# Kernel optimization log

Hardware: AMD Instinct MI355X
Metric: run time of the kernel (lower is better)

The kernel has to match this reference:

```python
import jax, jax.numpy as jnp
import numpy as np

N = 50000          # nodes
E = 800000         # edges (avg degree 16)
IN_C = 3
HEADS = 4
NUM_GRAPHS = 8
NUM_CLASSES = 10


def setup_inputs() -> dict:
    key = jax.random.key(0)
    ks = jax.random.split(key, 12)
    x = jax.random.normal(ks[0], (N, IN_C), jnp.float32)
    edge_index = jax.random.randint(ks[1], (2, E), 0, N, dtype=jnp.int64)
    batch = jnp.sort(jax.random.randint(ks[2], (N,), 0, NUM_GRAPHS, dtype=jnp.int64))

    def glorot(k, shape, fan):
        return jax.random.normal(k, shape, jnp.float32) * np.float32(1.0 / np.sqrt(fan))

    return {
        "x": x, "edge_index": edge_index, "batch": batch,
        "fc0_w": glorot(ks[3], (IN_C, 16), IN_C), "fc0_b": jnp.zeros((16,), jnp.float32),
        "u1": glorot(ks[4], (16, HEADS), 16), "c1": jnp.zeros((HEADS,), jnp.float32),
        "w1": glorot(ks[5], (16, HEADS * 32), 16), "b1": jnp.zeros((32,), jnp.float32),
        "u2": glorot(ks[6], (32, HEADS), 32), "c2": jnp.zeros((HEADS,), jnp.float32),
        "w2": glorot(ks[7], (32, HEADS * 64), 32), "b2": jnp.zeros((64,), jnp.float32),
        "fc1_w": glorot(ks[8], (64, NUM_CLASSES), 64), "fc1_b": jnp.zeros((NUM_CLASSES,), jnp.float32),
    }


def feast_conv(x, src, dst, u, c, w, b, heads, out_c):
    """FeaStConv (t_inv=True): per-edge head softmax on (x_j - x_i), mean aggregation."""
    n = x.shape[0]
    # soft-assignment over heads: [E, H]
    q = jax.nn.softmax((x[src] - x[dst]) @ u + c, axis=-1)
    # transform at node level, then gather per edge: [E, H, out_c]
    xw = (x @ w).reshape(n, heads, out_c)
    msg = jnp.einsum('eh,ehc->ec', q, xw[src])           # [E, out_c]
    agg = jax.ops.segment_sum(msg, dst, num_segments=n)  # sum over incoming edges
    cnt = jax.ops.segment_sum(jnp.ones((src.shape[0],), x.dtype), dst, num_segments=n)
    return agg / jnp.maximum(cnt, 1.0)[:, None] + b


def global_mean_pool(x, batch, num_graphs):
    s = jax.ops.segment_sum(x, batch, num_segments=num_graphs)
    cnt = jax.ops.segment_sum(jnp.ones((x.shape[0],), x.dtype), batch, num_segments=num_graphs)
    return s / jnp.maximum(cnt, 1.0)[:, None]


def reference(x, edge_index, batch, fc0_w, fc0_b, u1, c1, w1, b1, u2, c2, w2, b2, fc1_w, fc1_b):
    src, dst = edge_index[0], edge_index[1]   # x_j = x[src], x_i = x[dst]
    h = jax.nn.relu(x @ fc0_w + fc0_b)                              # [N, 16]
    h = jax.nn.relu(feast_conv(h, src, dst, u1, c1, w1, b1, HEADS, 32))  # [N, 32]
    h = jax.nn.relu(feast_conv(h, src, dst, u2, c2, w2, b2, HEADS, 64))  # [N, 64]
    g = global_mean_pool(h, batch, NUM_GRAPHS)                      # [G, 64]
    # dropout is identity in eval mode
    return g @ fc1_w + fc1_b                                        # [G, num_classes]
```

## Files before the change

kernel.cpp:

```cpp
#include <hip/hip_runtime.h>

#define N_NODES 50000
#define N_EDGES 800000
#define HEADS 4
#define NUM_GRAPHS 8

#define EBLK ((N_EDGES + 255) / 256)
#define NBLK ((N_NODES + 255) / 256)

__global__ __launch_bounds__(256) void hist_fc0_kernel(
    const int* __restrict__ dst, int* __restrict__ deg, int* __restrict__ off,
    const float* __restrict__ x,
    const float* __restrict__ fc0_w, const float* __restrict__ fc0_b,
    const float* __restrict__ u1,
    float* __restrict__ h0, float* __restrict__ P1) {
  if (blockIdx.x < EBLK) {
    int e = blockIdx.x * 256 + threadIdx.x;
    if (e < N_EDGES) off[e] = atomicAdd(&deg[dst[e]], 1);
    return;
  }
  __shared__ float sW0[3 * 16];
  __shared__ float sB0[16];
  __shared__ float sU[16 * 4];
  for (int i = threadIdx.x; i < 48; i += 256) sW0[i] = fc0_w[i];
  for (int i = threadIdx.x; i < 16; i += 256) sB0[i] = fc0_b[i];
  for (int i = threadIdx.x; i < 64; i += 256) sU[i] = u1[i];
  __syncthreads();
  int n = (blockIdx.x - EBLK) * 256 + threadIdx.x;
  if (n >= N_NODES) return;
  float x0 = x[n * 3 + 0], x1 = x[n * 3 + 1], x2 = x[n * 3 + 2];
  float h[16];
#pragma unroll
  for (int j = 0; j < 16; j++) {
    float v = x0 * sW0[0 * 16 + j] + x1 * sW0[1 * 16 + j] + x2 * sW0[2 * 16 + j] + sB0[j];
    h[j] = fmaxf(v, 0.f);
    h0[(size_t)n * 16 + j] = h[j];
  }
  float p0 = 0.f, p1 = 0.f, p2 = 0.f, p3 = 0.f;
#pragma unroll
  for (int j = 0; j < 16; j++) {
    p0 += h[j] * sU[j * 4 + 0];
    p1 += h[j] * sU[j * 4 + 1];
    p2 += h[j] * sU[j * 4 + 2];
    p3 += h[j] * sU[j * 4 + 3];
  }
  reinterpret_cast<float4*>(P1)[n] = make_float4(p0, p1, p2, p3);
}

__global__ __launch_bounds__(256) void alloc_kernel(const int* __restrict__ deg,
                                                    int* __restrict__ gctr,
                                                    int* __restrict__ rowstart) {
  int i = blockIdx.x * blockDim.x + threadIdx.x;
  int lane = threadIdx.x & 63;
  int d = (i < N_NODES) ? deg[i] : 0;
  int pre = d;
#pragma unroll
  for (int offd = 1; offd < 64; offd <<= 1) {
    int v = __shfl_up(pre, offd, 64);
    if (lane >= offd) pre += v;
  }
  int total = __shfl(pre, 63, 64);
  int base = 0;
  if (lane == 63) base = atomicAdd(gctr, total);
  base = __shfl(base, 63, 64);
  if (i < N_NODES) rowstart[i] = base + pre - d;
}

__global__ __launch_bounds__(256) void scatter_kernel(const int* __restrict__ src,
                                                      const int* __restrict__ dst,
                                                      const int* __restrict__ rowstart,
                                                      const int* __restrict__ off,
                                                      int* __restrict__ src_perm) {
  int e = blockIdx.x * blockDim.x + threadIdx.x;
  if (e >= N_EDGES) return;
  src_perm[rowstart[dst[e]] + off[e]] = src[e];
}

__device__ __forceinline__ float4 edge_q(float4 Ps, float b0, float b1, float b2, float b3) {
  float l0 = Ps.x + b0, l1 = Ps.y + b1, l2 = Ps.z + b2, l3 = Ps.w + b3;
  float m = fmaxf(fmaxf(l0, l1), fmaxf(l2, l3));
  float e0 = __expf(l0 - m), e1 = __expf(l1 - m), e2 = __expf(l2 - m), e3 = __expf(l3 - m);
  float inv = 1.f / (e0 + e1 + e2 + e3);
  return make_float4(e0 * inv, e1 * inv, e2 * inv, e3 * inv);
}

__global__ __launch_bounds__(256) void agg1_kernel(
    const int* __restrict__ rowstart, const int* __restrict__ deg,
    const int* __restrict__ src_perm,
    const float* __restrict__ P1, const float* __restrict__ c1,
    const float* __restrict__ h0,
    float* __restrict__ A) {
  int wave = threadIdx.x >> 6;
  int lane = threadIdx.x & 63;
  int g = lane >> 4;
  int j = lane & 15;
  int node = blockIdx.x * 4 + wave;
  if (node >= N_NODES) return;
  float4 Pd = reinterpret_cast<const float4*>(P1)[node];
  float b0 = c1[0] - Pd.x, b1 = c1[1] - Pd.y, b2 = c1[2] - Pd.z, b3 = c1[3] - Pd.w;
  int e0 = rowstart[node];
  int e1 = e0 + deg[node];
  const float4* P4 = reinterpret_cast<const float4*>(P1);
  float a0 = 0.f, a1 = 0.f, a2 = 0.f, a3 = 0.f;
  int p = e0;
  for (; p + 16 <= e1; p += 16) {
    int sA = src_perm[p + 0 + g];
    int sB = src_perm[p + 4 + g];
    int sC = src_perm[p + 8 + g];
    int sD = src_perm[p + 12 + g];
    float4 PA = P4[sA];
    float4 PB = P4[sB];
    float4 PC = P4[sC];
    float4 PD = P4[sD];
    float fA = h0[(size_t)sA * 16 + j];
    float fB = h0[(size_t)sB * 16 + j];
    float fC = h0[(size_t)sC * 16 + j];
    float fD = h0[(size_t)sD * 16 + j];
    float4 qA = edge_q(PA, b0, b1, b2, b3);
    float4 qB = edge_q(PB, b0, b1, b2, b3);
    float4 qC = edge_q(PC, b0, b1, b2, b3);
    float4 qD = edge_q(PD, b0, b1, b2, b3);
    a0 += qA.x * fA + qB.x * fB + qC.x * fC + qD.x * fD;
    a1 += qA.y * fA + qB.y * fB + qC.y * fC + qD.y * fD;
    a2 += qA.z * fA + qB.z * fB + qC.z * fC + qD.z * fD;
    a3 += qA.w * fA + qB.w * fB + qC.w * fC + qD.w * fD;
  }
  for (; p + 4 <= e1; p += 4) {
    int s = src_perm[p + g];
    float4 Ps = P4[s];
    float f = h0[(size_t)s * 16 + j];
    float4 q = edge_q(Ps, b0, b1, b2, b3);
    a0 += q.x * f; a1 += q.y * f; a2 += q.z * f; a3 += q.w * f;
  }
  int rem = e1 - p;
  if (g < rem) {
    int s = src_perm[p + g];
    float4 Ps = P4[s];
    float f = h0[(size_t)s * 16 + j];
    float4 q = edge_q(Ps, b0, b1, b2, b3);
    a0 += q.x * f; a1 += q.y * f; a2 += q.z * f; a3 += q.w * f;
  }
  a0 += __shfl_xor(a0, 16, 64); a0 += __shfl_xor(a0, 32, 64);
  a1 += __shfl_xor(a1, 16, 64); a1 += __shfl_xor(a1, 32, 64);
  a2 += __shfl_xor(a2, 16, 64); a2 += __shfl_xor(a2, 32, 64);
  a3 += __shfl_xor(a3, 16, 64); a3 += __shfl_xor(a3, 32, 64);
  float o = (g == 0) ? a0 : (g == 1) ? a1 : (g == 2) ? a2 : a3;
  A[(size_t)node * 64 + lane] = o;
}

__global__ __launch_bounds__(256) void agg2_kernel(
    const int* __restrict__ rowstart, const int* __restrict__ deg,
    const int* __restrict__ src_perm,
    const float* __restrict__ P2, const float* __restrict__ c2,
    const float* __restrict__ h1,
    float* __restrict__ A) {
  int wave = threadIdx.x >> 6;
  int lane = threadIdx.x & 63;
  int g = lane >> 5;
  int j = lane & 31;
  int node = blockIdx.x * 4 + wave;
  if (node >= N_NODES) return;
  float4 Pd = reinterpret_cast<const float4*>(P2)[node];
  float b0 = c2[0] - Pd.x, b1 = c2[1] - Pd.y, b2 = c2[2] - Pd.z, b3 = c2[3] - Pd.w;
  int e0 = rowstart[node];
  int e1 = e0 + deg[node];
  const float4* P4 = reinterpret_cast<const float4*>(P2);
  float a0 = 0.f, a1 = 0.f, a2 = 0.f, a3 = 0.f;
  int p = e0;
  for (; p + 8 <= e1; p += 8) {
    int sA = src_perm[p + 0 + g];
    int sB = src_perm[p + 2 + g];
    int sC = src_perm[p + 4 + g];
    int sD = src_perm[p + 6 + g];
    float4 PA = P4[sA];
    float4 PB = P4[sB];
    float4 PC = P4[sC];
    float4 PD = P4[sD];
    float fA = h1[(size_t)sA * 32 + j];
    float fB = h1[(size_t)sB * 32 + j];
    float fC = h1[(size_t)sC * 32 + j];
    float fD = h1[(size_t)sD * 32 + j];
    float4 qA = edge_q(PA, b0, b1, b2, b3);
    float4 qB = edge_q(PB, b0, b1, b2, b3);
    float4 qC = edge_q(PC, b0, b1, b2, b3);
    float4 qD = edge_q(PD, b0, b1, b2, b3);
    a0 += qA.x * fA + qB.x * fB + qC.x * fC + qD.x * fD;
    a1 += qA.y * fA + qB.y * fB + qC.y * fC + qD.y * fD;
    a2 += qA.z * fA + qB.z * fB + qC.z * fC + qD.z * fD;
    a3 += qA.w * fA + qB.w * fB + qC.w * fC + qD.w * fD;
  }
  for (; p + 2 <= e1; p += 2) {
    int s = src_perm[p + g];
    float4 Ps = P4[s];
    float f = h1[(size_t)s * 32 + j];
    float4 q = edge_q(Ps, b0, b1, b2, b3);
    a0 += q.x * f; a1 += q.y * f; a2 += q.z * f; a3 += q.w * f;
  }
  int rem = e1 - p;
  if (g < rem) {
    int s = src_perm[p + g];
    float4 Ps = P4[s];
    float f = h1[(size_t)s * 32 + j];
    float4 q = edge_q(Ps, b0, b1, b2, b3);
    a0 += q.x * f; a1 += q.y * f; a2 += q.z * f; a3 += q.w * f;
  }
  a0 += __shfl_xor(a0, 32, 64);
  a1 += __shfl_xor(a1, 32, 64);
  a2 += __shfl_xor(a2, 32, 64);
  a3 += __shfl_xor(a3, 32, 64);
  float oa = (g == 0) ? a0 : a1;
  float ob = (g == 0) ? a2 : a3;
  A[(size_t)node * 128 + lane] = oa;
  A[(size_t)node * 128 + 64 + lane] = ob;
}

__global__ __launch_bounds__(256) void gemm1_kernel(
    const int* __restrict__ deg, const float* __restrict__ A,
    const float* __restrict__ w1, const float* __restrict__ b1,
    const float* __restrict__ u2,
    float* __restrict__ h1, float* __restrict__ P2) {
  __shared__ float sB[64 * 32];
  __shared__ float sU[32 * 4];
  for (int i = threadIdx.x; i < 64 * 32; i += 256) {
    int hj = i / 32, c = i % 32;
    sB[i] = w1[(hj % 16) * 128 + (hj / 16) * 32 + c];
  }
  for (int i = threadIdx.x; i < 128; i += 256) sU[i] = u2[i];
  __syncthreads();
  const float4* sB4 = reinterpret_cast<const float4*>(sB);
  int c4 = threadIdx.x & 7;
  int g = threadIdx.x >> 3;
  int n0 = blockIdx.x * 64 + g * 2;
  int n1 = n0 + 1;
  int na = min(n0, N_NODES - 1);
  int nb = min(n1, N_NODES - 1);
  const float4* A0 = reinterpret_cast<const float4*>(A + (size_t)na * 64);
  const float4* A1 = reinterpret_cast<const float4*>(A + (size_t)nb * 64);
  float4 bc = reinterpret_cast<const float4*>(b1)[c4];
  float4 acc0 = {0, 0, 0, 0}, acc1 = {0, 0, 0, 0};
#pragma unroll 2
  for (int k4 = 0; k4 < 16; k4++) {
    float4 a0 = A0[k4];
    float4 a1 = A1[k4];
    float4 w0 = sB4[(4 * k4 + 0) * 8 + c4];
    float4 wv1 = sB4[(4 * k4 + 1) * 8 + c4];
    float4 w2v = sB4[(4 * k4 + 2) * 8 + c4];
    float4 w3 = sB4[(4 * k4 + 3) * 8 + c4];
    acc0.x += a0.x * w0.x + a0.y * wv1.x + a0.z * w2v.x + a0.w * w3.x;
    acc0.y += a0.x * w0.y + a0.y * wv1.y + a0.z * w2v.y + a0.w * w3.y;
    acc0.z += a0.x * w0.z + a0.y * wv1.z + a0.z * w2v.z + a0.w * w3.z;
    acc0.w += a0.x * w0.w + a0.y * wv1.w + a0.z * w2v.w + a0.w * w3.w;
    acc1.x += a1.x * w0.x + a1.y * wv1.x + a1.z * w2v.x + a1.w * w3.x;
    acc1.y += a1.x * w0.y + a1.y * wv1.y + a1.z * w2v.y + a1.w * w3.y;
    acc1.z += a1.x * w0.z + a1.y * wv1.z + a1.z * w2v.z + a1.w * w3.z;
    acc1.w += a1.x * w0.w + a1.y * wv1.w + a1.z * w2v.w + a1.w * w3.w;
  }
  float inv0 = 1.f / fmaxf((float)deg[na], 1.f);
  float inv1 = 1.f / fmaxf((float)deg[nb], 1.f);
  float4 o0 = {fmaxf(acc0.x * inv0 + bc.x, 0.f), fmaxf(acc0.y * inv0 + bc.y, 0.f),
               fmaxf(acc0.z * inv0 + bc.z, 0.f), fmaxf(acc0.w * inv0 + bc.w, 0.f)};
  float4 o1 = {fmaxf(acc1.x * inv1 + bc.x, 0.f), fmaxf(acc1.y * inv1 + bc.y, 0.f),
               fmaxf(acc1.z * inv1 + bc.z, 0.f), fmaxf(acc1.w * inv1 + bc.w, 0.f)};
  if (n0 < N_NODES) reinterpret_cast<float4*>(h1 + (size_t)n0 * 32)[c4] = o0;
  if (n1 < N_NODES) reinterpret_cast<float4*>(h1 + (size_t)n1 * 32)[c4] = o1;
  float pa[4] = {0, 0, 0, 0}, pb[4] = {0, 0, 0, 0};
#pragma unroll
  for (int k = 0; k < 4; k++) {
    int c = 4 * c4 + k;
    float v0 = k == 0 ? o0.x : k == 1 ? o0.y : k == 2 ? o0.z : o0.w;
    float v1 = k == 0 ? o1.x : k == 1 ? o1.y : k == 2 ? o1.z : o1.w;
#pragma unroll
    for (int hh = 0; hh < 4; hh++) {
      pa[hh] += v0 * sU[c * 4 + hh];
      pb[hh] += v1 * sU[c * 4 + hh];
    }
  }
#pragma unroll
  for (int msk = 1; msk <= 4; msk <<= 1) {
#pragma unroll
    for (int hh = 0; hh < 4; hh++) {
      pa[hh] += __shfl_xor(pa[hh], msk, 64);
      pb[hh] += __shfl_xor(pb[hh], msk, 64);
    }
  }
  if (c4 == 0) {
    if (n0 < N_NODES)
      reinterpret_cast<float4*>(P2)[n0] = make_float4(pa[0], pa[1], pa[2], pa[3]);
    if (n1 < N_NODES)
      reinterpret_cast<float4*>(P2)[n1] = make_float4(pb[0], pb[1], pb[2], pb[3]);
  }
}

__global__ __launch_bounds__(256) void gemm2_kernel(
    const int* __restrict__ deg, const float* __restrict__ A,
    const float* __restrict__ w2, const float* __restrict__ b2,
    float* __restrict__ h2) {
  __shared__ float sB[128 * 64];
  for (int i = threadIdx.x; i < 128 * 64; i += 256) {
    int hj = i / 64, c = i % 64;
    sB[i] = w2[(hj % 32) * 256 + (hj / 32) * 64 + c];
  }
  __syncthreads();
  const float4* sB4 = reinterpret_cast<const float4*>(sB);
  int c4 = threadIdx.x & 15;
  int g = threadIdx.x >> 4;
  int n0 = blockIdx.x * 32 + g * 2;
  int n1 = n0 + 1;
  int na = min(n0, N_NODES - 1);
  int nb = min(n1, N_NODES - 1);
  const float4* A0 = reinterpret_cast<const float4*>(A + (size_t)na * 128);
  const float4* A1 = reinterpret_cast<const float4*>(A + (size_t)nb * 128);
  float4 bc = reinterpret_cast<const float4*>(b2)[c4];
  float4 acc0 = {0, 0, 0, 0}, acc1 = {0, 0, 0, 0};
#pragma unroll 2
  for (int k4 = 0; k4 < 32; k4++) {
    float4 a0 = A0[k4];
    float4 a1 = A1[k4];
    float4 w0 = sB4[(4 * k4 + 0) * 16 + c4];
    float4 wv1 = sB4[(4 * k4 + 1) * 16 + c4];
    float4 w2v = sB4[(4 * k4 + 2) * 16 + c4];
    float4 w3 = sB4[(4 * k4 + 3) * 16 + c4];
    acc0.x += a0.x * w0.x + a0.y * wv1.x + a0.z * w2v.x + a0.w * w3.x;
    acc0.y += a0.x * w0.y + a0.y * wv1.y + a0.z * w2v.y + a0.w * w3.y;
    acc0.z += a0.x * w0.z + a0.y * wv1.z + a0.z * w2v.z + a0.w * w3.z;
    acc0.w += a0.x * w0.w + a0.y * wv1.w + a0.z * w2v.w + a0.w * w3.w;
    acc1.x += a1.x * w0.x + a1.y * wv1.x + a1.z * w2v.x + a1.w * w3.x;
    acc1.y += a1.x * w0.y + a1.y * wv1.y + a1.z * w2v.y + a1.w * w3.y;
    acc1.z += a1.x * w0.z + a1.y * wv1.z + a1.z * w2v.z + a1.w * w3.z;
    acc1.w += a1.x * w0.w + a1.y * wv1.w + a1.z * w2v.w + a1.w * w3.w;
  }
  if (n0 < N_NODES) {
    float inv = 1.f / fmaxf((float)deg[n0], 1.f);
    float4 o = {fmaxf(acc0.x * inv + bc.x, 0.f), fmaxf(acc0.y * inv + bc.y, 0.f),
                fmaxf(acc0.z * inv + bc.z, 0.f), fmaxf(acc0.w * inv + bc.w, 0.f)};
    reinterpret_cast<float4*>(h2 + (size_t)n0 * 64)[c4] = o;
  }
  if (n1 < N_NODES) {
    float inv = 1.f / fmaxf((float)deg[n1], 1.f);
    float4 o = {fmaxf(acc1.x * inv + bc.x, 0.f), fmaxf(acc1.y * inv + bc.y, 0.f),
                fmaxf(acc1.z * inv + bc.z, 0.f), fmaxf(acc1.w * inv + bc.w, 0.f)};
    reinterpret_cast<float4*>(h2 + (size_t)n1 * 64)[c4] = o;
  }
}

#define POOL_CHUNK 64
__global__ __launch_bounds__(256) void pool_kernel(
    const float* __restrict__ h2, const int* __restrict__ batch,
    float* __restrict__ gsum, float* __restrict__ gcnt) {
  int grp = threadIdx.x / 64;
  int c = threadIdx.x % 64;
  int n0 = (blockIdx.x * 4 + grp) * POOL_CHUNK;
  int n1 = min(n0 + POOL_CHUNK, N_NODES);
  if (n0 >= N_NODES) return;
  float acc = 0.f;
  float cacc = 0.f;
  int curg = batch[n0];
  for (int n = n0; n < n1; n++) {
    int g = batch[n];
    float v = h2[(size_t)n * 64 + c];
    if (g != curg) {
      atomicAdd(&gsum[curg * 64 + c], acc);
      if (c == 0) atomicAdd(&gcnt[curg], cacc);
      acc = 0.f;
      cacc = 0.f;
      curg = g;
    }
    acc += v;
    cacc += 1.f;
  }
  atomicAdd(&gsum[curg * 64 + c], acc);
  if (c == 0) atomicAdd(&gcnt[curg], cacc);
}

__global__ __launch_bounds__(128) void head_kernel(
    const float* __restrict__ gsum, const float* __restrict__ gcnt,
    const float* __restrict__ fc1_w, const float* __restrict__ fc1_b,
    float* __restrict__ out) {
  int t = threadIdx.x;
  if (t >= NUM_GRAPHS * 10) return;
  int g = t / 10, k = t % 10;
  float inv = 1.f / fmaxf(gcnt[g], 1.f);
  float s = fc1_b[k];
#pragma unroll
  for (int c = 0; c < 64; c++) s += gsum[g * 64 + c] * inv * fc1_w[c * 10 + k];
  out[g * 10 + k] = s;
}

extern "C" void kernel_launch(void* const* d_in, const int* in_sizes, int n_in,
                              void* d_out, int out_size, void* d_ws, size_t ws_size,
                              hipStream_t stream) {
  const float* x = (const float*)d_in[0];
  const int* edge_index = (const int*)d_in[1];
  const int* batch = (const int*)d_in[2];
  const float* fc0_w = (const float*)d_in[3];
  const float* fc0_b = (const float*)d_in[4];
  const float* u1 = (const float*)d_in[5];
  const float* c1 = (const float*)d_in[6];
  const float* w1 = (const float*)d_in[7];
  const float* b1 = (const float*)d_in[8];
  const float* u2 = (const float*)d_in[9];
  const float* c2 = (const float*)d_in[10];
  const float* w2 = (const float*)d_in[11];
  const float* b2 = (const float*)d_in[12];
  const float* fc1_w = (const float*)d_in[13];
  const float* fc1_b = (const float*)d_in[14];
  float* out = (float*)d_out;

  const int* src = edge_index;
  const int* dst = edge_index + N_EDGES;

  char* wsb = (char*)d_ws;
  int* deg = (int*)wsb;
  int* gctr = deg + N_NODES;
  float* gsum = (float*)wsb + 50004;
  float* gcnt = gsum + NUM_GRAPHS * 64;
  int* rowstart = (int*)wsb + 50524;
  int* off = rowstart + N_NODES;
  int* src_perm = off + N_EDGES;
  float* h0 = (float*)wsb + 1700524;
  float* h1 = h0 + (size_t)N_NODES * 16;
  float* h2 = h1 + (size_t)N_NODES * 32;
  float* A = h2 + (size_t)N_NODES * 64;
  float* P1 = A + (size_t)N_NODES * 128;
  float* P2 = P1 + (size_t)N_NODES * 4;

  hipMemsetAsync(d_ws, 0, 50524 * sizeof(int), stream);

  int nblk = NBLK;
  int eblk = EBLK;
  int wblk = (N_NODES + 3) / 4;

  hist_fc0_kernel<<<eblk + nblk, 256, 0, stream>>>(dst, deg, off, x, fc0_w, fc0_b, u1, h0, P1);
  alloc_kernel<<<nblk, 256, 0, stream>>>(deg, gctr, rowstart);
  scatter_kernel<<<eblk, 256, 0, stream>>>(src, dst, rowstart, off, src_perm);

  agg1_kernel<<<wblk, 256, 0, stream>>>(rowstart, deg, src_perm, P1, c1, h0, A);
  gemm1_kernel<<<(N_NODES + 63) / 64, 256, 0, stream>>>(deg, A, w1, b1, u2, h1, P2);

  agg2_kernel<<<wblk, 256, 0, stream>>>(rowstart, deg, src_perm, P2, c2, h1, A);
  gemm2_kernel<<<(N_NODES + 31) / 32, 256, 0, stream>>>(deg, A, w2, b2, h2);

  int pblk = (N_NODES + POOL_CHUNK * 4 - 1) / (POOL_CHUNK * 4);
  pool_kernel<<<pblk, 256, 0, stream>>>(h2, batch, gsum, gcnt);
  head_kernel<<<1, 128, 0, stream>>>(gsum, gcnt, fc1_w, fc1_b, out);
}
```

Baseline: 275.3 us.

## Remap aggregation lanes to more edges per wave with float4 feature loads

Both aggregation kernels now assign each lane a float4 slice of the source feature row, so a wave covers 16 edges (agg1) or 8 edges (agg2) per step instead of 4 or 2. Feature gathers become 16-byte vector loads and the per-edge softmax is computed by fewer redundant lanes. The cost is a longer cross-lane shuffle reduction over 16 float accumulators, more register use, and idle lanes for low-degree nodes when the edge count is below the wider step.

After: 277.9 us. About the same (+0.9%).

```diff
diff --git a/kernel.cpp b/kernel.cpp
--- a/kernel.cpp
+++ b/kernel.cpp
@@ -84,6 +84,17 @@
   return make_float4(e0 * inv, e1 * inv, e2 * inv, e3 * inv);
 }
 
+__device__ __forceinline__ void fma4(float4& a, float s, const float4& f) {
+  a.x += s * f.x; a.y += s * f.y; a.z += s * f.z; a.w += s * f.w;
+}
+
+__device__ __forceinline__ void red4(float4& a, int m) {
+  a.x += __shfl_xor(a.x, m, 64);
+  a.y += __shfl_xor(a.y, m, 64);
+  a.z += __shfl_xor(a.z, m, 64);
+  a.w += __shfl_xor(a.w, m, 64);
+}
+
 __global__ __launch_bounds__(256) void agg1_kernel(
     const int* __restrict__ rowstart, const int* __restrict__ deg,
     const int* __restrict__ src_perm,
@@ -92,8 +103,8 @@
     float* __restrict__ A) {
   int wave = threadIdx.x >> 6;
   int lane = threadIdx.x & 63;
-  int g = lane >> 4;
-  int j = lane & 15;
+  int g = lane >> 2;
+  int jj = lane & 3;
   int node = blockIdx.x * 4 + wave;
   if (node >= N_NODES) return;
   float4 Pd = reinterpret_cast<const float4*>(P1)[node];
@@ -101,51 +112,37 @@
   int e0 = rowstart[node];
   int e1 = e0 + deg[node];
   const float4* P4 = reinterpret_cast<const float4*>(P1);
-  float a0 = 0.f, a1 = 0.f, a2 = 0.f, a3 = 0.f;
+  float4 aH0 = {0, 0, 0, 0}, aH1 = {0, 0, 0, 0}, aH2 = {0, 0, 0, 0}, aH3 = {0, 0, 0, 0};
   int p = e0;
   for (; p + 16 <= e1; p += 16) {
-    int sA = src_perm[p + 0 + g];
-    int sB = src_perm[p + 4 + g];
-    int sC = src_perm[p + 8 + g];
-    int sD = src_perm[p + 12 + g];
-    float4 PA = P4[sA];
-    float4 PB = P4[sB];
-    float4 PC = P4[sC];
-    float4 PD = P4[sD];
-    float fA = h0[(size_t)sA * 16 + j];
-    float fB = h0[(size_t)sB * 16 + j];
-    float fC = h0[(size_t)sC * 16 + j];
-    float fD = h0[(size_t)sD * 16 + j];
-    float4 qA = edge_q(PA, b0, b1, b2, b3);
-    float4 qB = edge_q(PB, b0, b1, b2, b3);
-    float4 qC = edge_q(PC, b0, b1, b2, b3);
-    float4 qD = edge_q(PD, b0, b1, b2, b3);
-    a0 += qA.x * fA + qB.x * fB + qC.x * fC + qD.x * fD;
-    a1 += qA.y * fA + qB.y * fB + qC.y * fC + qD.y * fD;
-    a2 += qA.z * fA + qB.z * fB + qC.z * fC + qD.z * fD;
-    a3 += qA.w * fA + qB.w * fB + qC.w * fC + qD.w * fD;
-  }
-  for (; p + 4 <= e1; p += 4) {
     int s = src_perm[p + g];
     float4 Ps = P4[s];
-    float f = h0[(size_t)s * 16 + j];
+    float4 f = *reinterpret_cast<const float4*>(h0 + (size_t)s * 16 + 4 * jj);
     float4 q = edge_q(Ps, b0, b1, b2, b3);
-    a0 += q.x * f; a1 += q.y * f; a2 += q.z * f; a3 += q.w * f;
+    fma4(aH0, q.x, f);
+    fma4(aH1, q.y, f);
+    fma4(aH2, q.z, f);
+    fma4(aH3, q.w, f);
   }
   int rem = e1 - p;
   if (g < rem) {
     int s = src_perm[p + g];
     float4 Ps = P4[s];
-    float f = h0[(size_t)s * 16 + j];
+    float4 f = *reinterpret_cast<const float4*>(h0 + (size_t)s * 16 + 4 * jj);
     float4 q = edge_q(Ps, b0, b1, b2, b3);
-    a0 += q.x * f; a1 += q.y * f; a2 += q.z * f; a3 += q.w * f;
-  }
-  a0 += __shfl_xor(a0, 16, 64); a0 += __shfl_xor(a0, 32, 64);
-  a1 += __shfl_xor(a1, 16, 64); a1 += __shfl_xor(a1, 32, 64);
-  a2 += __shfl_xor(a2, 16, 64); a2 += __shfl_xor(a2, 32, 64);
-  a3 += __shfl_xor(a3, 16, 64); a3 += __shfl_xor(a3, 32, 64);
-  float o = (g == 0) ? a0 : (g == 1) ? a1 : (g == 2) ? a2 : a3;
-  A[(size_t)node * 64 + lane] = o;
+    fma4(aH0, q.x, f);
+    fma4(aH1, q.y, f);
+    fma4(aH2, q.z, f);
+    fma4(aH3, q.w, f);
+  }
+#pragma unroll
+  for (int m = 4; m <= 32; m <<= 1) {
+    red4(aH0, m); red4(aH1, m); red4(aH2, m); red4(aH3, m);
+  }
+  if (g < 4) {
+    float4 v = (g == 0) ? aH0 : (g == 1) ? aH1 : (g == 2) ? aH2 : aH3;
+    *reinterpret_cast<float4*>(A + (size_t)node * 64 + g * 16 + 4 * jj) = v;
+  }
 }
 
 __global__ __launch_bounds__(256) void agg2_kernel(
@@ -156,8 +153,8 @@
     float* __restrict__ A) {
   int wave = threadIdx.x >> 6;
   int lane = threadIdx.x & 63;
-  int g = lane >> 5;
-  int j = lane & 31;
+  int g = lane >> 3;
+  int jj = lane & 7;
   int node = blockIdx.x * 4 + wave;
   if (node >= N_NODES) return;
   float4 Pd = reinterpret_cast<const float4*>(P2)[node];
@@ -165,53 +162,51 @@
   int e0 = rowstart[node];
   int e1 = e0 + deg[node];
   const float4* P4 = reinterpret_cast<const float4*>(P2);
-  float a0 = 0.f, a1 = 0.f, a2 = 0.f, a3 = 0.f;
+  float4 aH0 = {0, 0, 0, 0}, aH1 = {0, 0, 0, 0}, aH2 = {0, 0, 0, 0}, aH3 = {0, 0, 0, 0};
   int p = e0;
-  for (; p + 8 <= e1; p += 8) {
-    int sA = src_perm[p + 0 + g];
-    int sB = src_perm[p + 2 + g];
-    int sC = src_perm[p + 4 + g];
-    int sD = src_perm[p + 6 + g];
+  for (; p + 16 <= e1; p += 16) {
+    int sA = src_perm[p + g];
+    int sB = src_perm[p + 8 + g];
     float4 PA = P4[sA];
     float4 PB = P4[sB];
-    float4 PC = P4[sC];
-    float4 PD = P4[sD];
-    float fA = h1[(size_t)sA * 32 + j];
-    float fB = h1[(size_t)sB * 32 + j];
-    float fC = h1[(size_t)sC * 32 + j];
-    float fD = h1[(size_t)sD * 32 + j];
+    float4 fA = *reinterpret_cast<const float4*>(h1 + (size_t)sA * 32 + 4 * jj);
+    float4 fB = *reinterpret_cast<const float4*>(h1 + (size_t)sB * 32 + 4 * jj);
     float4 qA = edge_q(PA, b0, b1, b2, b3);
     float4 qB = edge_q(PB, b0, b1, b2, b3);
-    float4 qC = edge_q(PC, b0, b1, b2, b3);
-    float4 qD = edge_q(PD, b0, b1, b2, b3);
-    a0 += qA.x * fA + qB.x * fB + qC.x * fC + qD.x * fD;
-    a1 += qA.y * fA + qB.y * fB + qC.y * fC + qD.y * fD;
-    a2 += qA.z * fA + qB.z * fB + qC.z * fC + qD.z * fD;
-    a3 += qA.w * fA + qB.w * fB + qC.w * fC + qD.w * fD;
-  }
-  for (; p + 2 <= e1; p += 2) {
+    fma4(aH0, qA.x, fA); fma4(aH0, qB.x, fB);
+    fma4(aH1, qA.y, fA); fma4(aH1, qB.y, fB);
+    fma4(aH2, qA.z, fA); fma4(aH2, qB.z, fB);
+    fma4(aH3, qA.w, fA); fma4(aH3, qB.w, fB);
+  }
+  for (; p + 8 <= e1; p += 8) {
     int s = src_perm[p + g];
     float4 Ps = P4[s];
-    float f = h1[(size_t)s * 32 + j];
+    float4 f = *reinterpret_cast<const float4*>(h1 + (size_t)s * 32 + 4 * jj);
     float4 q = edge_q(Ps, b0, b1, b2, b3);
-    a0 += q.x * f; a1 += q.y * f; a2 += q.z * f; a3 += q.w * f;
+    fma4(aH0, q.x, f);
+    fma4(aH1, q.y, f);
+    fma4(aH2, q.z, f);
+    fma4(aH3, q.w, f);
   }
   int rem = e1 - p;
   if (g < rem) {
     int s = src_perm[p + g];
     float4 Ps = P4[s];
-    float f = h1[(size_t)s * 32 + j];
+    float4 f = *reinterpret_cast<const float4*>(h1 + (size_t)s * 32 + 4 * jj);
     float4 q = edge_q(Ps, b0, b1, b2, b3);
-    a0 += q.x * f; a1 += q.y * f; a2 += q.z * f; a3 += q.w * f;
-  }
-  a0 += __shfl_xor(a0, 32, 64);
-  a1 += __shfl_xor(a1, 32, 64);
-  a2 += __shfl_xor(a2, 32, 64);
-  a3 += __shfl_xor(a3, 32, 64);
-  float oa = (g == 0) ? a0 : a1;
-  float ob = (g == 0) ? a2 : a3;
-  A[(size_t)node * 128 + lane] = oa;
-  A[(size_t)node * 128 + 64 + lane] = ob;
+    fma4(aH0, q.x, f);
+    fma4(aH1, q.y, f);
+    fma4(aH2, q.z, f);
+    fma4(aH3, q.w, f);
+  }
+#pragma unroll
+  for (int m = 8; m <= 32; m <<= 1) {
+    red4(aH0, m); red4(aH1, m); red4(aH2, m); red4(aH3, m);
+  }
+  if (g < 4) {
+    float4 v = (g == 0) ? aH0 : (g == 1) ? aH1 : (g == 2) ? aH2 : aH3;
+    *reinterpret_cast<float4*>(A + (size_t)node * 128 + g * 32 + 4 * jj) = v;
+  }
 }
 
 __global__ __launch_bounds__(256) void gemm1_kernel(
```
